# Kernel optimization log

Measured on AMD Instinct MI355X. Metric: run time of the kernel, lower is better.

The kernel has to match this reference:

```python
import jax, jax.numpy as jnp
import numpy as np

N, NFEAT, NHID, NCLASS = 10000, 512, 64, 10
ALPHA = 0.2


def setup_inputs() -> dict:
    key = jax.random.key(0)
    ks = jax.random.split(key, 8)
    x = jax.random.normal(ks[0], (N, NFEAT), dtype=jnp.float32)
    adj1 = jax.random.uniform(ks[1], (N, N), dtype=jnp.float32) / N  # row-normalized-ish
    adj2 = jax.random.uniform(ks[2], (N, N), dtype=jnp.float32) / N
    # GraphConvolution params (glorot-ish scale)
    W1 = jax.random.normal(ks[3], (NFEAT, NHID), dtype=jnp.float32) * (1.0 / np.sqrt(NFEAT))
    b1 = jnp.zeros((NHID,), dtype=jnp.float32)
    W2 = jax.random.normal(ks[4], (NFEAT, NHID), dtype=jnp.float32) * (1.0 / np.sqrt(NFEAT))
    b2 = jnp.zeros((NHID,), dtype=jnp.float32)
    attn_w = jax.random.normal(ks[5], (NHID, 1), dtype=jnp.float32) * (1.0 / np.sqrt(NHID))
    cluster = jax.random.normal(ks[6], (NCLASS, NHID), dtype=jnp.float32)
    return {"x": x, "adj1": adj1, "adj2": adj2, "W1": W1, "b1": b1,
            "W2": W2, "b2": b2, "attn_w": attn_w, "cluster": cluster}


def reference(x, adj1, adj2, W1, b1, W2, b2, attn_w, cluster):
    # Two GCN branches: output = adj @ (x @ W) + b
    emb1 = adj1 @ (x @ W1) + b1  # [N, H]
    emb2 = adj2 @ (x @ W2) + b2  # [N, H]
    z = jnp.stack([emb1, emb2], axis=1)            # [N, 2, H]
    # tiny 2-way attention fusion
    w = z @ attn_w                                  # [N, 2, 1]
    beta = jax.nn.softmax(w, axis=1)                # softmax over the 2 views
    emb = jnp.sum(beta * z, axis=1)                 # [N, H]
    # DEC cluster assignment (faithful to the original, including the
    # second power and the /2, which the row-normalization cancels)
    d2 = jnp.sum((emb[:, None, :] - cluster[None, :, :]) ** 2, axis=2)  # [N, K]
    q = 1.0 / (1.0 + d2 / ALPHA)
    q = q ** ((ALPHA + 1.0) / 2.0)
    q = q ** (ALPHA + 1.0) / 2.0
    q = q / jnp.sum(q, axis=1, keepdims=True)
    return emb, q
```

## Files before the change

kernel.cpp:

```cpp
#include <hip/hip_runtime.h>
#include <math.h>

#define NROWS 10000
#define FEAT  512
#define NHID  64
#define NCLS  10
#define YT_STRIDE 10240
#define KB_PAD 320
#define TK    64
#define NSPLIT 5
#define NT    32

typedef __attribute__((ext_vector_type(8))) short short8;
typedef __attribute__((ext_vector_type(4))) float f32x4;

__device__ __forceinline__ short f2bf(float f) {
  union { float f; unsigned u; } v; v.f = f;
  unsigned r = v.u + 0x7fffu + ((v.u >> 16) & 1u);
  return (short)(r >> 16);
}

__device__ __forceinline__ float wsum64(float v) {
#pragma unroll
  for (int off = 32; off > 0; off >>= 1) v += __shfl_xor(v, off, 64);
  return v;
}

__device__ __forceinline__ void gload16(const void* g, void* l) {
  __builtin_amdgcn_global_load_lds(
      (const __attribute__((address_space(1))) unsigned int*)g,
      (__attribute__((address_space(3))) unsigned int*)l, 16, 0, 0);
}

__global__ __launch_bounds__(256) void prep_w(const float* __restrict__ W1,
                                              const float* __restrict__ W2,
                                              unsigned short* __restrict__ Wt1,
                                              unsigned short* __restrict__ Wt2) {
  int i = blockIdx.x * 256 + threadIdx.x;
  if (i >= FEAT * NHID) return;
  int k = i >> 6, h = i & 63;
  Wt1[h * FEAT + k] = (unsigned short)f2bf(W1[i]);
  Wt2[h * FEAT + k] = (unsigned short)f2bf(W2[i]);
}

__global__ __launch_bounds__(256) void gemm_xw(const float* __restrict__ x,
                                               const unsigned short* __restrict__ Wt1,
                                               const unsigned short* __restrict__ Wt2,
                                               unsigned short* __restrict__ Yt1,
                                               unsigned short* __restrict__ Yt2) {
  const int lane = threadIdx.x & 63;
  const int wave = threadIdx.x >> 6;
  const int job = blockIdx.x * 4 + wave;
  if (job >= 1250) return;
  const int br = (job >= 625) ? 1 : 0;
  const int tile = job - 625 * br;
  const unsigned short* Wt = br ? Wt2 : Wt1;
  unsigned short* Yt       = br ? Yt2 : Yt1;
  const int rowbase = tile * 16;
  const int r16 = lane & 15, g = lane >> 4, ga = g * 8;

  const float* arow = x + (size_t)(rowbase + r16) * FEAT + ga;
  const unsigned short* bp = Wt + (size_t)r16 * FEAT + ga;

  f32x4 acc[4];
#pragma unroll
  for (int t = 0; t < 4; ++t) acc[t] = (f32x4){0.f, 0.f, 0.f, 0.f};

#pragma unroll
  for (int kb = 0; kb < FEAT / 32; ++kb) {
    const int k0 = kb * 32;
    const f32x4* ap = (const f32x4*)(arow + k0);
    f32x4 a0 = ap[0], a1 = ap[1];
    short8 af;
    af[0] = f2bf(a0[0]); af[1] = f2bf(a0[1]); af[2] = f2bf(a0[2]); af[3] = f2bf(a0[3]);
    af[4] = f2bf(a1[0]); af[5] = f2bf(a1[1]); af[6] = f2bf(a1[2]); af[7] = f2bf(a1[3]);
#pragma unroll
    for (int t = 0; t < 4; ++t) {
      short8 bf = *(const short8*)(bp + (size_t)t * 16 * FEAT + k0);
      acc[t] = __builtin_amdgcn_mfma_f32_16x16x32_bf16(af, bf, acc[t], 0, 0, 0);
    }
  }
  const int sw = (r16 & 7) << 3;
#pragma unroll
  for (int t = 0; t < 4; ++t)
#pragma unroll
    for (int rr = 0; rr < 4; ++rr) {
      const int col = t * 16 + r16;
      const int row = rowbase + g * 4 + rr;
      Yt[(size_t)col * YT_STRIDE + (row ^ sw)] = (unsigned short)f2bf(acc[t][rr]);
    }
}

__global__ __launch_bounds__(256, 3) void gemm_adj(const float* __restrict__ adj1,
                                                   const float* __restrict__ adj2,
                                                   const unsigned short* __restrict__ Yt1,
                                                   const unsigned short* __restrict__ Yt2,
                                                   float* __restrict__ Ep) {
  __shared__ __attribute__((aligned(16))) float          Asm[2][64 * TK];
  __shared__ __attribute__((aligned(16))) unsigned short Bsm[2][64 * TK];

  const int sp = blockIdx.y;
  const int br = blockIdx.z;
  const float* adj         = br ? adj2 : adj1;
  const unsigned short* Yt = br ? Yt2 : Yt1;
  float* E = Ep + (size_t)(br * NSPLIT + sp) * NROWS * NHID;
  const int k_base = sp * (NT * TK);
  const int blockrow = blockIdx.x * 64;

  const int lane = threadIdx.x & 63;
  const int wave = threadIdx.x >> 6;

  const int a_rt_l = (lane >> 4);
  const int a_gran = (lane & 15) * 4;
  const int b_cl = lane >> 3;
  const int b_el = (lane & 7) * 8;

  const int wr = wave >> 1, wc = wave & 1;
  const int r16 = lane & 15, g = lane >> 4;
  const int aswz = (r16 & 7) << 2;
  const int swb  = (r16 & 7) << 3;

  f32x4 acc00 = (f32x4){0.f, 0.f, 0.f, 0.f};
  f32x4 acc01 = acc00, acc10 = acc00, acc11 = acc00;

#define STAGE(tt) { const int k0s = k_base + (tt) * TK; const int bufs = (tt) & 1;   \
    _Pragma("unroll")                                                                 \
    for (int j = 0; j < 4; ++j) {                                                     \
      const int rt = wave * 16 + j * 4 + a_rt_l;                                      \
      const int gr = min(blockrow + rt, NROWS - 1);                                   \
      const int fsrc = a_gran ^ ((rt & 7) << 2);                                      \
      const float* asrc = adj + (size_t)gr * NROWS + min(k0s + fsrc, NROWS - 4);      \
      gload16(asrc, &Asm[bufs][(wave * 16 + j * 4) * TK]);                            \
    }                                                                                 \
    _Pragma("unroll")                                                                 \
    for (int j = 0; j < 2; ++j) {                                                     \
      const int c0 = wave * 16 + j * 8;                                               \
      const unsigned short* bsrc =                                                    \
          Yt + (size_t)(c0 + b_cl) * YT_STRIDE + (k0s + b_el);                        \
      gload16(bsrc, &Bsm[bufs][c0 * TK]);                                             \
    } }

#define COMPUTE(tt) { const int bufc = (tt) & 1;                                      \
    _Pragma("unroll")                                                                 \
    for (int ks = 0; ks < 2; ++ks) {                                                  \
      const int kx = ks * 32 + g * 8;                                                 \
      const float* ab0 = &Asm[bufc][(wr * 32 + r16) * TK];                            \
      const float* ab1 = &Asm[bufc][(wr * 32 + 16 + r16) * TK];                       \
      f32x4 a00 = *(const f32x4*)(ab0 + (kx ^ aswz));                                 \
      f32x4 a01 = *(const f32x4*)(ab0 + ((kx + 4) ^ aswz));                           \
      f32x4 a10 = *(const f32x4*)(ab1 + (kx ^ aswz));                                 \
      f32x4 a11 = *(const f32x4*)(ab1 + ((kx + 4) ^ aswz));                           \
      short8 b0 = *(const short8*)&Bsm[bufc][(wc * 32 + r16) * TK + (kx ^ swb)];      \
      short8 b1 = *(const short8*)&Bsm[bufc][(wc * 32 + 16 + r16) * TK + (kx ^ swb)]; \
      short8 af0, af1;                                                                \
      af0[0] = f2bf(a00[0]); af0[1] = f2bf(a00[1]); af0[2] = f2bf(a00[2]);            \
      af0[3] = f2bf(a00[3]); af0[4] = f2bf(a01[0]); af0[5] = f2bf(a01[1]);            \
      af0[6] = f2bf(a01[2]); af0[7] = f2bf(a01[3]);                                   \
      af1[0] = f2bf(a10[0]); af1[1] = f2bf(a10[1]); af1[2] = f2bf(a10[2]);            \
      af1[3] = f2bf(a10[3]); af1[4] = f2bf(a11[0]); af1[5] = f2bf(a11[1]);            \
      af1[6] = f2bf(a11[2]); af1[7] = f2bf(a11[3]);                                   \
      acc00 = __builtin_amdgcn_mfma_f32_16x16x32_bf16(af0, b0, acc00, 0, 0, 0);       \
      acc01 = __builtin_amdgcn_mfma_f32_16x16x32_bf16(af0, b1, acc01, 0, 0, 0);       \
      acc10 = __builtin_amdgcn_mfma_f32_16x16x32_bf16(af1, b0, acc10, 0, 0, 0);       \
      acc11 = __builtin_amdgcn_mfma_f32_16x16x32_bf16(af1, b1, acc11, 0, 0, 0);       \
    } }

  STAGE(0);
#pragma unroll 2
  for (int t = 0; t < NT - 1; ++t) {
    STAGE(t + 1);
    asm volatile("s_waitcnt vmcnt(6)" ::: "memory");
    __builtin_amdgcn_sched_barrier(0);
    __builtin_amdgcn_s_barrier();
    __builtin_amdgcn_sched_barrier(0);
    COMPUTE(t);
    __builtin_amdgcn_s_barrier();
  }
  asm volatile("s_waitcnt vmcnt(0)" ::: "memory");
  __builtin_amdgcn_sched_barrier(0);
  __builtin_amdgcn_s_barrier();
  __builtin_amdgcn_sched_barrier(0);
  COMPUTE(NT - 1);
#undef STAGE
#undef COMPUTE

#pragma unroll
  for (int rr = 0; rr < 4; ++rr) {
    const int grow0 = blockrow + wr * 32 + g * 4 + rr;
    const int grow1 = grow0 + 16;
    const int col   = wc * 32 + r16;
    if (grow0 < NROWS) {
      float* e = E + (size_t)grow0 * NHID + col;
      e[0]  = acc00[rr];
      e[16] = acc01[rr];
    }
    if (grow1 < NROWS) {
      float* e = E + (size_t)grow1 * NHID + col;
      e[0]  = acc10[rr];
      e[16] = acc11[rr];
    }
  }
}

__global__ __launch_bounds__(256) void gemm_adj_dyn(const float* __restrict__ adj1,
                                                    const float* __restrict__ adj2,
                                                    const unsigned short* __restrict__ Yt1,
                                                    const unsigned short* __restrict__ Yt2,
                                                    float* __restrict__ Ep,
                                                    int nsplit, int chunk) {
  const int sp = blockIdx.y;
  const int br = blockIdx.z;
  const float* adj          = br ? adj2 : adj1;
  const unsigned short* Yt  = br ? Yt2 : Yt1;
  float* E = Ep + (size_t)(br * nsplit + sp) * NROWS * NHID;

  const int kb_begin = sp * chunk;
  const int kb_end   = min(kb_begin + chunk, KB_PAD);

  const int lane = threadIdx.x & 63;
  const int wave = threadIdx.x >> 6;
  const int rowbase = blockIdx.x * 64 + wave * 16;
  if (rowbase >= NROWS) return;
  const int r = lane & 15;
  const int g = lane >> 4;
  const int ga = g * 8;
  const int sw = (r & 7) << 3;

  const float* arow = adj + (size_t)(rowbase + r) * NROWS;

  f32x4 acc0 = (f32x4){0.f, 0.f, 0.f, 0.f};
  f32x4 acc1 = acc0, acc2 = acc0, acc3 = acc0;

#pragma unroll 4
  for (int kb = kb_begin; kb < kb_end; ++kb) {
    const int k0 = kb * 32;
    const int kc = min(k0 + ga, 9992);
    const int ks = (k0 + ga) ^ sw;
    const f32x4* ap = (const f32x4*)(arow + kc);
    f32x4 a0 = ap[0], a1 = ap[1];
    short8 af;
    af[0] = f2bf(a0[0]); af[1] = f2bf(a0[1]); af[2] = f2bf(a0[2]); af[3] = f2bf(a0[3]);
    af[4] = f2bf(a1[0]); af[5] = f2bf(a1[1]); af[6] = f2bf(a1[2]); af[7] = f2bf(a1[3]);
    short8 bf0 = *(const short8*)(Yt + (size_t)(0 * 16 + r) * YT_STRIDE + ks);
    short8 bf1 = *(const short8*)(Yt + (size_t)(1 * 16 + r) * YT_STRIDE + ks);
    short8 bf2 = *(const short8*)(Yt + (size_t)(2 * 16 + r) * YT_STRIDE + ks);
    short8 bf3 = *(const short8*)(Yt + (size_t)(3 * 16 + r) * YT_STRIDE + ks);
    acc0 = __builtin_amdgcn_mfma_f32_16x16x32_bf16(af, bf0, acc0, 0, 0, 0);
    acc1 = __builtin_amdgcn_mfma_f32_16x16x32_bf16(af, bf1, acc1, 0, 0, 0);
    acc2 = __builtin_amdgcn_mfma_f32_16x16x32_bf16(af, bf2, acc2, 0, 0, 0);
    acc3 = __builtin_amdgcn_mfma_f32_16x16x32_bf16(af, bf3, acc3, 0, 0, 0);
  }

  const size_t ebase = (size_t)(rowbase + g * 4) * NHID + r;
#pragma unroll
  for (int rr = 0; rr < 4; ++rr) {
    E[ebase + (size_t)rr * NHID +  0] = acc0[rr];
    E[ebase + (size_t)rr * NHID + 16] = acc1[rr];
    E[ebase + (size_t)rr * NHID + 32] = acc2[rr];
    E[ebase + (size_t)rr * NHID + 48] = acc3[rr];
  }
}

__global__ __launch_bounds__(256) void fuse(const float* __restrict__ Ep,
                                            int nsplit,
                                            const float* __restrict__ b1,
                                            const float* __restrict__ b2,
                                            const float* __restrict__ aw,
                                            const float* __restrict__ cl,
                                            float* __restrict__ out) {
  const int lane = threadIdx.x & 63;
  const int wave = threadIdx.x >> 6;
  const int row = blockIdx.x * 4 + wave;
  if (row >= NROWS) return;

  const size_t off = (size_t)row * NHID + lane;
  const size_t bstride = (size_t)nsplit * NROWS * NHID;
  float e1 = b1[lane], e2 = b2[lane];
  for (int s = 0; s < nsplit; ++s) {
    e1 += Ep[(size_t)s * NROWS * NHID + off];
    e2 += Ep[bstride + (size_t)s * NROWS * NHID + off];
  }

  float a = aw[lane];
  float w1 = wsum64(e1 * a);
  float w2 = wsum64(e2 * a);
  float m = fmaxf(w1, w2);
  float x1 = expf(w1 - m), x2 = expf(w2 - m);
  float inv = 1.0f / (x1 + x2);
  float emb = (x1 * e1 + x2 * e2) * inv;
  out[off] = emb;

  float myq = 0.f, qs = 0.f;
#pragma unroll
  for (int c = 0; c < NCLS; ++c) {
    float d = emb - cl[c * NHID + lane];
    float s = wsum64(d * d);
    float t = exp2f(-0.72f * log2f(fmaf(5.0f, s, 1.0f)));
    qs += t;
    if (lane == c) myq = t;
  }
  if (lane < NCLS) out[(size_t)NROWS * NHID + (size_t)row * NCLS + lane] = myq / qs;
}

extern "C" void kernel_launch(void* const* d_in, const int* in_sizes, int n_in,
                              void* d_out, int out_size, void* d_ws, size_t ws_size,
                              hipStream_t stream) {
  const float* x    = (const float*)d_in[0];
  const float* adj1 = (const float*)d_in[1];
  const float* adj2 = (const float*)d_in[2];
  const float* W1   = (const float*)d_in[3];
  const float* b1   = (const float*)d_in[4];
  const float* W2   = (const float*)d_in[5];
  const float* b2   = (const float*)d_in[6];
  const float* aw   = (const float*)d_in[7];
  const float* cl   = (const float*)d_in[8];
  float* out = (float*)d_out;

  char* ws = (char*)d_ws;
  unsigned short* Yt1 = (unsigned short*)(ws + 0);
  unsigned short* Yt2 = (unsigned short*)(ws + 1310720);
  unsigned short* Wt1 = (unsigned short*)(ws + 2621440);
  unsigned short* Wt2 = (unsigned short*)(ws + 2686976);
  float* Ep           = (float*)(ws + 2752512);

  const size_t fixed = 2752512;
  const size_t per_split = 2ull * NROWS * NHID * 4ull;
  const bool static_ok = ws_size >= fixed + (size_t)NSPLIT * per_split;

  hipMemsetAsync(Yt1, 0, 2 * 1310720, stream);
  prep_w<<<dim3(128), dim3(256), 0, stream>>>(W1, W2, Wt1, Wt2);
  gemm_xw<<<dim3(313), dim3(256), 0, stream>>>(x, Wt1, Wt2, Yt1, Yt2);

  if (static_ok) {
    gemm_adj<<<dim3(157, NSPLIT, 2), dim3(256), 0, stream>>>(adj1, adj2, Yt1, Yt2, Ep);
    fuse<<<dim3(2500), dim3(256), 0, stream>>>(Ep, NSPLIT, b1, b2, aw, cl, out);
  } else {
    int nsplit = 1;
    if (ws_size > fixed + per_split) {
      size_t s = (ws_size - fixed) / per_split;
      nsplit = (int)(s < 5 ? s : 5);
      if (nsplit < 1) nsplit = 1;
    }
    const int chunk = (KB_PAD + nsplit - 1) / nsplit;
    gemm_adj_dyn<<<dim3(157, nsplit, 2), dim3(256), 0, stream>>>(adj1, adj2, Yt1, Yt2,
                                                                 Ep, nsplit, chunk);
    fuse<<<dim3(2500), dim3(256), 0, stream>>>(Ep, nsplit, b1, b2, aw, cl, out);
  }
}
```

Before: 232.9 us.

## Enlarge adj GEMM tile to 128 rows with each wave owning full columns

Raises the adjacency GEMM block tile from 64 to 128 rows. Each wave now computes 32 rows across all 64 output columns, so every B fragment read from LDS feeds two MFMAs and there is no longer a 2x2 wave split. The A staging loads double, the vmcnt wait is raised to match, the grid is halved, and occupancy is lowered to 2 blocks per CU. The kernel is bound by streaming adj from memory, so fewer blocks (790) and lower occupancy may reduce latency hiding while trimming only the redundant B traffic.

```diff
diff --git a/kernel.cpp b/kernel.cpp
--- a/kernel.cpp
+++ b/kernel.cpp
@@ -8,6 +8,7 @@
 #define YT_STRIDE 10240
 #define KB_PAD 320
 #define TK    64
+#define TM    128
 #define NSPLIT 5
 #define NT    32
 
@@ -91,12 +92,12 @@
     }
 }
 
-__global__ __launch_bounds__(256, 3) void gemm_adj(const float* __restrict__ adj1,
+__global__ __launch_bounds__(256, 2) void gemm_adj(const float* __restrict__ adj1,
                                                    const float* __restrict__ adj2,
                                                    const unsigned short* __restrict__ Yt1,
                                                    const unsigned short* __restrict__ Yt2,
                                                    float* __restrict__ Ep) {
-  __shared__ __attribute__((aligned(16))) float          Asm[2][64 * TK];
+  __shared__ __attribute__((aligned(16))) float          Asm[2][TM * TK];
   __shared__ __attribute__((aligned(16))) unsigned short Bsm[2][64 * TK];
 
   const int sp = blockIdx.y;
@@ -105,32 +106,36 @@
   const unsigned short* Yt = br ? Yt2 : Yt1;
   float* E = Ep + (size_t)(br * NSPLIT + sp) * NROWS * NHID;
   const int k_base = sp * (NT * TK);
-  const int blockrow = blockIdx.x * 64;
+  const int blockrow = blockIdx.x * TM;
 
   const int lane = threadIdx.x & 63;
   const int wave = threadIdx.x >> 6;
 
-  const int a_rt_l = (lane >> 4);
+  const int a_rt_l = lane >> 4;
   const int a_gran = (lane & 15) * 4;
   const int b_cl = lane >> 3;
   const int b_el = (lane & 7) * 8;
 
-  const int wr = wave >> 1, wc = wave & 1;
   const int r16 = lane & 15, g = lane >> 4;
   const int aswz = (r16 & 7) << 2;
   const int swb  = (r16 & 7) << 3;
 
-  f32x4 acc00 = (f32x4){0.f, 0.f, 0.f, 0.f};
-  f32x4 acc01 = acc00, acc10 = acc00, acc11 = acc00;
+  f32x4 acc0[4], acc1[4];
+#pragma unroll
+  for (int t = 0; t < 4; ++t) {
+    acc0[t] = (f32x4){0.f, 0.f, 0.f, 0.f};
+    acc1[t] = (f32x4){0.f, 0.f, 0.f, 0.f};
+  }
 
 #define STAGE(tt) { const int k0s = k_base + (tt) * TK; const int bufs = (tt) & 1;   \
     _Pragma("unroll")                                                                 \
-    for (int j = 0; j < 4; ++j) {                                                     \
-      const int rt = wave * 16 + j * 4 + a_rt_l;                                      \
+    for (int j = 0; j < 8; ++j) {                                                     \
+      const int rtb = wave * 32 + j * 4;                                              \
+      const int rt = rtb + a_rt_l;                                                    \
       const int gr = min(blockrow + rt, NROWS - 1);                                   \
       const int fsrc = a_gran ^ ((rt & 7) << 2);                                      \
       const float* asrc = adj + (size_t)gr * NROWS + min(k0s + fsrc, NROWS - 4);      \
-      gload16(asrc, &Asm[bufs][(wave * 16 + j * 4) * TK]);                            \
+      gload16(asrc, &Asm[bufs][rtb * TK]);                                            \
     }                                                                                 \
     _Pragma("unroll")                                                                 \
     for (int j = 0; j < 2; ++j) {                                                     \
@@ -141,17 +146,15 @@
     } }
 
 #define COMPUTE(tt) { const int bufc = (tt) & 1;                                      \
+    const float* ab0 = &Asm[bufc][(wave * 32 + r16) * TK];                            \
+    const float* ab1 = &Asm[bufc][(wave * 32 + 16 + r16) * TK];                       \
     _Pragma("unroll")                                                                 \
     for (int ks = 0; ks < 2; ++ks) {                                                  \
       const int kx = ks * 32 + g * 8;                                                 \
-      const float* ab0 = &Asm[bufc][(wr * 32 + r16) * TK];                            \
-      const float* ab1 = &Asm[bufc][(wr * 32 + 16 + r16) * TK];                       \
       f32x4 a00 = *(const f32x4*)(ab0 + (kx ^ aswz));                                 \
       f32x4 a01 = *(const f32x4*)(ab0 + ((kx + 4) ^ aswz));                           \
       f32x4 a10 = *(const f32x4*)(ab1 + (kx ^ aswz));                                 \
       f32x4 a11 = *(const f32x4*)(ab1 + ((kx + 4) ^ aswz));                           \
-      short8 b0 = *(const short8*)&Bsm[bufc][(wc * 32 + r16) * TK + (kx ^ swb)];      \
-      short8 b1 = *(const short8*)&Bsm[bufc][(wc * 32 + 16 + r16) * TK + (kx ^ swb)]; \
       short8 af0, af1;                                                                \
       af0[0] = f2bf(a00[0]); af0[1] = f2bf(a00[1]); af0[2] = f2bf(a00[2]);            \
       af0[3] = f2bf(a00[3]); af0[4] = f2bf(a01[0]); af0[5] = f2bf(a01[1]);            \
@@ -159,17 +162,19 @@
       af1[0] = f2bf(a10[0]); af1[1] = f2bf(a10[1]); af1[2] = f2bf(a10[2]);            \
       af1[3] = f2bf(a10[3]); af1[4] = f2bf(a11[0]); af1[5] = f2bf(a11[1]);            \
       af1[6] = f2bf(a11[2]); af1[7] = f2bf(a11[3]);                                   \
-      acc00 = __builtin_amdgcn_mfma_f32_16x16x32_bf16(af0, b0, acc00, 0, 0, 0);       \
-      acc01 = __builtin_amdgcn_mfma_f32_16x16x32_bf16(af0, b1, acc01, 0, 0, 0);       \
-      acc10 = __builtin_amdgcn_mfma_f32_16x16x32_bf16(af1, b0, acc10, 0, 0, 0);       \
-      acc11 = __builtin_amdgcn_mfma_f32_16x16x32_bf16(af1, b1, acc11, 0, 0, 0);       \
+      _Pragma("unroll")                                                               \
+      for (int ct = 0; ct < 4; ++ct) {                                                \
+        short8 b = *(const short8*)&Bsm[bufc][(ct * 16 + r16) * TK + (kx ^ swb)];     \
+        acc0[ct] = __builtin_amdgcn_mfma_f32_16x16x32_bf16(af0, b, acc0[ct], 0, 0, 0);\
+        acc1[ct] = __builtin_amdgcn_mfma_f32_16x16x32_bf16(af1, b, acc1[ct], 0, 0, 0);\
+      }                                                                               \
     } }
 
   STAGE(0);
 #pragma unroll 2
   for (int t = 0; t < NT - 1; ++t) {
     STAGE(t + 1);
-    asm volatile("s_waitcnt vmcnt(6)" ::: "memory");
+    asm volatile("s_waitcnt vmcnt(10)" ::: "memory");
     __builtin_amdgcn_sched_barrier(0);
     __builtin_amdgcn_s_barrier();
     __builtin_amdgcn_sched_barrier(0);
@@ -185,21 +190,15 @@
 #undef COMPUTE
 
 #pragma unroll
-  for (int rr = 0; rr < 4; ++rr) {
-    const int grow0 = blockrow + wr * 32 + g * 4 + rr;
-    const int grow1 = grow0 + 16;
-    const int col   = wc * 32 + r16;
-    if (grow0 < NROWS) {
-      float* e = E + (size_t)grow0 * NHID + col;
-      e[0]  = acc00[rr];
-      e[16] = acc01[rr];
+  for (int ct = 0; ct < 4; ++ct)
+#pragma unroll
+    for (int rr = 0; rr < 4; ++rr) {
+      const int grow0 = blockrow + wave * 32 + g * 4 + rr;
+      const int grow1 = grow0 + 16;
+      const int col   = ct * 16 + r16;
+      if (grow0 < NROWS) E[(size_t)grow0 * NHID + col] = acc0[ct][rr];
+      if (grow1 < NROWS) E[(size_t)grow1 * NHID + col] = acc1[ct][rr];
     }
-    if (grow1 < NROWS) {
-      float* e = E + (size_t)grow1 * NHID + col;
-      e[0]  = acc10[rr];
-      e[16] = acc11[rr];
-    }
-  }
 }
 
 __global__ __launch_bounds__(256) void gemm_adj_dyn(const float* __restrict__ adj1,
@@ -332,7 +331,7 @@
   gemm_xw<<<dim3(313), dim3(256), 0, stream>>>(x, Wt1, Wt2, Yt1, Yt2);
 
   if (static_ok) {
-    gemm_adj<<<dim3(157, NSPLIT, 2), dim3(256), 0, stream>>>(adj1, adj2, Yt1, Yt2, Ep);
+    gemm_adj<<<dim3(79, NSPLIT, 2), dim3(256), 0, stream>>>(adj1, adj2, Yt1, Yt2, Ep);
     fuse<<<dim3(2500), dim3(256), 0, stream>>>(Ep, NSPLIT, b1, b2, aw, cl, out);
   } else {
     int nsplit = 1;
```

Result: faster. 224.0 us (-3.8%).
